# Kernel optimization log

Hardware: AMD Instinct MI355X
Metric: run time of the kernel (lower is better)

Reference implementation:

```python
import jax, jax.numpy as jnp
import numpy as np

N_NODES = 131072
IN_F = 512
HID = 512
H = 8
DH = HID // H
B = 1024  # batch_size (num graphs); static for jit
LN_EPS = 1e-5


def setup_inputs() -> dict:
    key = jax.random.key(0)
    ks = jax.random.split(key, 12)
    # equal-size segments (128 nodes/graph), sorted as in PyG batching
    batch = (jnp.arange(N_NODES) // (N_NODES // B)).astype(jnp.int32)
    s = 0.02
    return {
        "x": jax.random.normal(ks[0], (N_NODES, IN_F), jnp.float32),
        "batch": batch,
        "query": jax.random.normal(ks[1], (H, DH), jnp.float32) * s,
        "key_w": jax.random.normal(ks[2], (HID, IN_F), jnp.float32) * s,
        "key_b": jnp.zeros((HID,), jnp.float32),
        "value_w": jax.random.normal(ks[3], (HID, IN_F), jnp.float32) * s,
        "value_b": jnp.zeros((HID,), jnp.float32),
        "out_w": jax.random.normal(ks[4], (IN_F, HID), jnp.float32) * s,
        "out_b": jnp.zeros((IN_F,), jnp.float32),
        "gate_w": jax.random.normal(ks[5], (IN_F, 2 * IN_F), jnp.float32) * s,
        "gate_b": jnp.zeros((IN_F,), jnp.float32),
        "ln_w": jnp.ones((IN_F,), jnp.float32),
        "ln_b": jnp.zeros((IN_F,), jnp.float32),
    }


def reference(x, batch, query, key_w, key_b, value_w, value_b, out_w, out_b,
              gate_w, gate_b, ln_w, ln_b):
    N = x.shape[0]
    # projections (dense GEMMs)
    keys = (x @ key_w.T + key_b).reshape(N, H, DH)
    values = (x @ value_w.T + value_b).reshape(N, H, DH)
    # per-node attention logits against shared per-head query: [N, H]
    scores = jnp.einsum('nhd,hd->nh', keys, query)
    # segment softmax over nodes within each graph
    smax = jax.ops.segment_max(scores, batch, num_segments=B)  # [B, H]
    smax = jnp.where(jnp.isfinite(smax), smax, 0.0)            # guard empty graphs
    e = jnp.exp(scores - smax[batch])
    ssum = jax.ops.segment_sum(e, batch, num_segments=B)       # [B, H]
    w = e / jnp.maximum(ssum[batch], 1e-12)                    # [N, H]  (dropout is eval-mode identity)
    # attention-weighted pooling of values: [B, H, DH] -> [B, HID]
    pooled = jax.ops.segment_sum(w[:, :, None] * values, batch, num_segments=B)
    ctx = pooled.reshape(B, HID) @ out_w.T + out_b             # [B, IN_F]
    # gating with per-graph mean pool
    counts = jax.ops.segment_sum(jnp.ones((N,), x.dtype), batch, num_segments=B)
    avg = jax.ops.segment_sum(x, batch, num_segments=B) / jnp.maximum(counts, 1.0)[:, None]
    gate = jax.nn.sigmoid(jnp.concatenate([ctx, avg], axis=1) @ gate_w.T + gate_b)
    ctx = gate * ctx + (1.0 - gate) * avg
    emb = jnp.where(counts[:, None] > 0, ctx, 0.0)             # empty graphs stay zero
    # LayerNorm
    mu = emb.mean(-1, keepdims=True)
    var = emb.var(-1, keepdims=True)
    return (emb - mu) / jnp.sqrt(var + LN_EPS) * ln_w + ln_b
```

## Files before the change

### kernel.cpp

```cpp
#include <hip/hip_runtime.h>
#include <hip/hip_bf16.h>

typedef short short8 __attribute__((ext_vector_type(8)));
typedef float f32x4 __attribute__((ext_vector_type(4)));

#define NGRAPH 1024
#define NPG    128
#define INF    512
#define NHEAD  8

__device__ __forceinline__ ushort f2b(float f){
  __hip_bfloat16 h(f);
  union { __hip_bfloat16 h; ushort u; } v; v.h = h; return v.u;
}
__device__ __forceinline__ float b2f_lo(unsigned u){
  union { unsigned u; float f; } v; v.u = u << 16; return v.f;
}
__device__ __forceinline__ float b2f_hi(unsigned u){
  union { unsigned u; float f; } v; v.u = u & 0xffff0000u; return v.f;
}

__global__ void k_prep(const float* __restrict__ q, const float* __restrict__ kw,
                       float* __restrict__ kq,
                       const float* __restrict__ vw, ushort* __restrict__ vwb,
                       const float* __restrict__ ow, ushort* __restrict__ owb,
                       const float* __restrict__ gw, ushort* __restrict__ gwb){
  const int b = blockIdx.x, t = threadIdx.x;
  if(b < 16){
    int h = b >> 1, f = (b & 1)*256 + t;
    float s = 0.f;
    #pragma unroll 8
    for(int d = 0; d < 64; d++)
      s += q[h*64 + d] * kw[(size_t)(h*64 + d)*INF + f];
    kq[h*INF + f] = s;
  } else if(b < 16 + 1024){
    int i = (b - 16)*256 + t;   vwb[i] = f2b(vw[i]);
  } else if(b < 16 + 2048){
    int i = (b - 1040)*256 + t; owb[i] = f2b(ow[i]);
  } else {
    int i = (b - 2064)*256 + t; gwb[i] = f2b(gw[i]);
  }
}

__global__ __launch_bounds__(256, 2) void k_graph(
    const float* __restrict__ x, const float* __restrict__ kq,
    ushort* __restrict__ xw_b, float* __restrict__ avg_f, ushort* __restrict__ avg_b){
  __shared__ __align__(16) ushort xs[64*INF];
  __shared__ __align__(16) float  sc[64*NHEAD];
  __shared__ float mE[2*NHEAD];
  __shared__ float fD[2*NHEAD];

  const int t = threadIdx.x, lane = t & 63, w = t >> 6;
  const int col = lane & 15, kg = lane >> 4;
  const int g = blockIdx.x;
  const int node = w*16 + col;

  short8 bfrag[16];
  {
    const bool ok = (col < 8);
    const float* kqr = kq + col*INF;
    #pragma unroll
    for(int ks = 0; ks < 16; ks++){
      short8 v = short8{0,0,0,0,0,0,0,0};
      if(ok){
        float4 p0 = *(const float4*)(kqr + ks*32 + kg*8);
        float4 p1 = *(const float4*)(kqr + ks*32 + kg*8 + 4);
        v[0]=(short)f2b(p0.x); v[1]=(short)f2b(p0.y); v[2]=(short)f2b(p0.z); v[3]=(short)f2b(p0.w);
        v[4]=(short)f2b(p1.x); v[5]=(short)f2b(p1.y); v[6]=(short)f2b(p1.z); v[7]=(short)f2b(p1.w);
      }
      bfrag[ks] = v;
    }
  }

  float acc[2][NHEAD][2];
  #pragma unroll
  for(int c = 0; c < 2; c++)
    #pragma unroll
    for(int h = 0; h < NHEAD; h++){ acc[c][h][0] = 0.f; acc[c][h][1] = 0.f; }
  float cs0 = 0.f, cs1 = 0.f;

  #pragma unroll
  for(int c = 0; c < 2; c++){
    {
      const float* xr = x + (size_t)(g*NPG + c*64 + node)*INF + kg*8;
      f32x4 sacc = {0.f,0.f,0.f,0.f};
      #pragma unroll
      for(int ks = 0; ks < 16; ks++){
        float4 a = *(const float4*)(xr + ks*32);
        float4 b = *(const float4*)(xr + ks*32 + 4);
        short8 af;
        af[0]=(short)f2b(a.x); af[1]=(short)f2b(a.y); af[2]=(short)f2b(a.z); af[3]=(short)f2b(a.w);
        af[4]=(short)f2b(b.x); af[5]=(short)f2b(b.y); af[6]=(short)f2b(b.z); af[7]=(short)f2b(b.w);
        *(short8*)((char*)xs + node*1024 + ((ks*64 + kg*16) ^ ((node & 7) << 4))) = af;
        sacc = __builtin_amdgcn_mfma_f32_16x16x32_bf16(af, bfrag[ks], sacc, 0, 0, 0);
      }
      if(col < 8){
        #pragma unroll
        for(int r = 0; r < 4; r++)
          sc[(w*16 + kg*4 + r)*NHEAD + col] = sacc[r];
      }
    }
    __syncthreads();

    if(t < 128){
      int h = t >> 4, s = t & 15;
      float v[4]; float m = -1e30f;
      #pragma unroll
      for(int i = 0; i < 4; i++){ v[i] = sc[(s + 16*i)*NHEAD + h]; m = fmaxf(m, v[i]); }
      #pragma unroll
      for(int msk = 1; msk < 16; msk <<= 1) m = fmaxf(m, __shfl_xor(m, msk));
      float es = 0.f;
      #pragma unroll
      for(int i = 0; i < 4; i++){ v[i] = __expf(v[i] - m); es += v[i]; }
      #pragma unroll
      for(int msk = 1; msk < 16; msk <<= 1) es += __shfl_xor(es, msk);
      if(c == 0){
        #pragma unroll
        for(int i = 0; i < 4; i++) sc[(s + 16*i)*NHEAD + h] = v[i];
        if(s == 0){ mE[h] = m; mE[8 + h] = es; }
      } else {
        float m0 = mE[h], E0 = mE[8 + h];
        float M  = fmaxf(m0, m);
        float f1 = __expf(m - M);
        #pragma unroll
        for(int i = 0; i < 4; i++) sc[(s + 16*i)*NHEAD + h] = v[i]*f1;
        if(s == 0){
          float f0 = __expf(m0 - M);
          float D  = f0*E0 + f1*es;
          fD[h] = f0; fD[8 + h] = 1.0f / fmaxf(D, 1e-12f);
        }
      }
    }
    __syncthreads();

    #pragma unroll 4
    for(int n = 0; n < 64; n++){
      unsigned xv = *(const unsigned*)((const char*)xs + n*1024 + ((4*t) ^ ((n & 7) << 4)));
      float x0 = b2f_lo(xv), x1 = b2f_hi(xv);
      float4 w0 = *(float4*)(sc + n*NHEAD);
      float4 w1 = *(float4*)(sc + n*NHEAD + 4);
      float wv[8] = {w0.x, w0.y, w0.z, w0.w, w1.x, w1.y, w1.z, w1.w};
      #pragma unroll
      for(int h = 0; h < NHEAD; h++){
        acc[c][h][0] += wv[h]*x0;
        acc[c][h][1] += wv[h]*x1;
      }
      cs0 += x0; cs1 += x1;
    }
    __syncthreads();
  }

  #pragma unroll
  for(int h = 0; h < NHEAD; h++){
    float f0 = fD[h], dinv = fD[8 + h];
    float v0 = (f0*acc[0][h][0] + acc[1][h][0]) * dinv;
    float v1 = (f0*acc[0][h][1] + acc[1][h][1]) * dinv;
    unsigned pk = (unsigned)f2b(v0) | ((unsigned)f2b(v1) << 16);
    *(unsigned*)(xw_b + (size_t)g*4096 + h*INF + 2*t) = pk;
  }
  float am0 = cs0*(1.0f/128.0f), am1 = cs1*(1.0f/128.0f);
  float2 av = {am0, am1};
  *(float2*)(avg_f + (size_t)g*INF + 2*t) = av;
  unsigned pk = (unsigned)f2b(am0) | ((unsigned)f2b(am1) << 16);
  *(unsigned*)(avg_b + (size_t)g*INF + 2*t) = pk;
}

__global__ __launch_bounds__(256, 2) void gemm_tn(
    const ushort* __restrict__ A1, const ushort* __restrict__ A2,
    int lda, int headmode,
    const ushort* __restrict__ Wt, int ldw,
    const float* __restrict__ bias,
    float* __restrict__ Cf, ushort* __restrict__ Cb,
    int ldc, int K, int ksplit){
  __shared__ ushort As[2][64*40];
  __shared__ ushort Bs[2][64*40];
  const int t = threadIdx.x, lane = t & 63, w = t >> 6;
  const int m0 = blockIdx.x*64, n0 = blockIdx.y*64;
  const int aoff = headmode ? blockIdx.y*512 : 0;
  const int col = lane & 15, kg = lane >> 4;
  const int lr = t >> 2, lk = (t & 3)*8;

  f32x4 acc[2][2];
  #pragma unroll
  for(int i = 0; i < 2; i++)
    #pragma unroll
    for(int j = 0; j < 2; j++) acc[i][j] = f32x4{0.f,0.f,0.f,0.f};

  const ushort* Ap0 = (0 < ksplit) ? A1 : A2;
  short8 va = *(const short8*)(Ap0 + (size_t)(m0 + lr)*lda + aoff + lk);
  short8 vb = *(const short8*)(Wt + (size_t)(n0 + lr)*ldw + lk);
  int buf = 0;
  for(int kc = 0; kc < K; kc += 32){
    *(short8*)((char*)&As[buf][0] + lr*80 + lk*2) = va;
    *(short8*)((char*)&Bs[buf][0] + lr*80 + lk*2) = vb;
    __syncthreads();
    if(kc + 32 < K){
      int kn = kc + 32;
      const ushort* Ap = (kn < ksplit) ? A1 : A2;
      int kl = (kn < ksplit) ? kn : kn - ksplit;
      va = *(const short8*)(Ap + (size_t)(m0 + lr)*lda + aoff + kl + lk);
      vb = *(const short8*)(Wt + (size_t)(n0 + lr)*ldw + kn + lk);
    }
    const int mr = (w & 1)*32, nc = (w >> 1)*32;
    short8 af0 = *(short8*)((char*)&As[buf][0] + (mr + col)*80 + kg*16);
    short8 af1 = *(short8*)((char*)&As[buf][0] + (mr + 16 + col)*80 + kg*16);
    short8 bf0 = *(short8*)((char*)&Bs[buf][0] + (nc + col)*80 + kg*16);
    short8 bf1 = *(short8*)((char*)&Bs[buf][0] + (nc + 16 + col)*80 + kg*16);
    acc[0][0] = __builtin_amdgcn_mfma_f32_16x16x32_bf16(af0, bf0, acc[0][0], 0,0,0);
    acc[0][1] = __builtin_amdgcn_mfma_f32_16x16x32_bf16(af0, bf1, acc[0][1], 0,0,0);
    acc[1][0] = __builtin_amdgcn_mfma_f32_16x16x32_bf16(af1, bf0, acc[1][0], 0,0,0);
    acc[1][1] = __builtin_amdgcn_mfma_f32_16x16x32_bf16(af1, bf1, acc[1][1], 0,0,0);
    buf ^= 1;
  }
  #pragma unroll
  for(int mi = 0; mi < 2; mi++)
    #pragma unroll
    for(int ni = 0; ni < 2; ni++)
      #pragma unroll
      for(int r = 0; r < 4; r++){
        int rr = m0 + (w & 1)*32 + mi*16 + kg*4 + r;
        int cc = n0 + (w >> 1)*32 + ni*16 + col;
        float vv = acc[mi][ni][r] + bias[cc];
        if(Cf) Cf[(size_t)rr*ldc + cc] = vv;
        if(Cb) Cb[(size_t)rr*ldc + cc] = f2b(vv);
      }
}

__global__ __launch_bounds__(512, 2) void k5_epilogue(
    const float* __restrict__ z, const float* __restrict__ ctx,
    const float* __restrict__ avg, const float* __restrict__ lnw,
    const float* __restrict__ lnb, float* __restrict__ out){
  __shared__ float red[16];
  const int t = threadIdx.x, b = blockIdx.x;
  const size_t i = (size_t)b*INF + t;
  float zz = z[i], c = ctx[i], a = avg[i];
  float g = 1.0f / (1.0f + __expf(-zz));
  float e = g*c + (1.0f - g)*a;
  float s1 = e, s2 = e*e;
  #pragma unroll
  for(int m = 1; m < 64; m <<= 1){ s1 += __shfl_xor(s1, m); s2 += __shfl_xor(s2, m); }
  int wv = t >> 6;
  if((t & 63) == 0){ red[wv] = s1; red[8 + wv] = s2; }
  __syncthreads();
  float ts1 = 0.f, ts2 = 0.f;
  #pragma unroll
  for(int k = 0; k < 8; k++){ ts1 += red[k]; ts2 += red[8 + k]; }
  float mu = ts1 * (1.0f/512.0f);
  float var = ts2 * (1.0f/512.0f) - mu*mu;
  out[i] = (e - mu) * rsqrtf(var + 1e-5f) * lnw[t] + lnb[t];
}

extern "C" void kernel_launch(void* const* d_in, const int* in_sizes, int n_in,
                              void* d_out, int out_size, void* d_ws, size_t ws_size,
                              hipStream_t stream){
  const float* x       = (const float*)d_in[0];
  const float* query   = (const float*)d_in[2];
  const float* key_w   = (const float*)d_in[3];
  const float* value_w = (const float*)d_in[5];
  const float* value_b = (const float*)d_in[6];
  const float* out_w   = (const float*)d_in[7];
  const float* out_b   = (const float*)d_in[8];
  const float* gate_w  = (const float*)d_in[9];
  const float* gate_b  = (const float*)d_in[10];
  const float* ln_w    = (const float*)d_in[11];
  const float* ln_b    = (const float*)d_in[12];
  float* out = (float*)d_out;

  char* ws = (char*)d_ws;
  float*  kq       = (float*) (ws + 0);
  ushort* vw_b     = (ushort*)(ws + 16384);
  ushort* ow_b     = (ushort*)(ws + 540672);
  ushort* gw_b     = (ushort*)(ws + 1064960);
  ushort* xw_b     = (ushort*)(ws + 2113536);
  float*  avg_f    = (float*) (ws + 10502144);
  ushort* avg_b    = (ushort*)(ws + 12599296);
  ushort* pooled_b = (ushort*)(ws + 13647872);
  float*  ctx_f    = (float*) (ws + 14696448);
  ushort* ctx_b    = (ushort*)(ws + 16793600);
  float*  z_f      = (float*) (ws + 17842176);

  k_prep<<<4112, 256, 0, stream>>>(query, key_w, kq, value_w, vw_b,
                                   out_w, ow_b, gate_w, gw_b);

  k_graph<<<NGRAPH, 256, 0, stream>>>(x, kq, xw_b, avg_f, avg_b);

  gemm_tn<<<dim3(16, 8), 256, 0, stream>>>(xw_b, xw_b, 4096, 1, vw_b, 512, value_b,
                                           nullptr, pooled_b, 512, 512, 1 << 30);
  gemm_tn<<<dim3(16, 8), 256, 0, stream>>>(pooled_b, pooled_b, 512, 0, ow_b, 512, out_b,
                                           ctx_f, ctx_b, 512, 512, 1 << 30);
  gemm_tn<<<dim3(16, 8), 256, 0, stream>>>(ctx_b, avg_b, 512, 0, gw_b, 1024, gate_b,
                                           z_f, nullptr, 512, 1024, 512);

  k5_epilogue<<<NGRAPH, 512, 0, stream>>>(z_f, ctx_f, avg_f, ln_w, ln_b, out);
}
```

Measured before the change: 112.0 us.

## Shrink graph kernel to 128 threads with online softmax over 32-node chunks; deepen GEMM K-step

The per-graph kernel now runs 128 threads and walks the 128 nodes in four 32-node chunks. Its softmax becomes a running online rescale across chunks, so the shared staging buffer shrinks and more blocks can fit per CU. Each thread now accumulates four feature columns instead of two. Separately, the GEMM consumes 64 K-elements per shared-memory stage instead of 32, which halves the number of barriers. The trade-offs are more serial chunk iterations, fewer threads loading x per block, and higher register pressure.

```diff
diff --git a/kernel.cpp b/kernel.cpp
--- a/kernel.cpp
+++ b/kernel.cpp
@@ -8,6 +8,7 @@
 #define NPG    128
 #define INF    512
 #define NHEAD  8
+#define CH     32
 
 __device__ __forceinline__ ushort f2b(float f){
   __hip_bfloat16 h(f);
@@ -42,13 +43,12 @@
   }
 }
 
-__global__ __launch_bounds__(256, 2) void k_graph(
+__global__ __launch_bounds__(128, 2) void k_graph(
     const float* __restrict__ x, const float* __restrict__ kq,
     ushort* __restrict__ xw_b, float* __restrict__ avg_f, ushort* __restrict__ avg_b){
-  __shared__ __align__(16) ushort xs[64*INF];
-  __shared__ __align__(16) float  sc[64*NHEAD];
-  __shared__ float mE[2*NHEAD];
-  __shared__ float fD[2*NHEAD];
+  __shared__ __align__(16) ushort xs[CH*INF];
+  __shared__ __align__(16) float  sc[CH*NHEAD];
+  __shared__ float mEf[3*NHEAD];
 
   const int t = threadIdx.x, lane = t & 63, w = t >> 6;
   const int col = lane & 15, kg = lane >> 4;
@@ -72,17 +72,18 @@
     }
   }
 
-  float acc[2][NHEAD][2];
-  #pragma unroll
-  for(int c = 0; c < 2; c++)
-    #pragma unroll
-    for(int h = 0; h < NHEAD; h++){ acc[c][h][0] = 0.f; acc[c][h][1] = 0.f; }
-  float cs0 = 0.f, cs1 = 0.f;
-
-  #pragma unroll
-  for(int c = 0; c < 2; c++){
+  if(t < NHEAD){ mEf[t] = -1e30f; mEf[NHEAD + t] = 0.f; }
+
+  float acc[NHEAD][4];
+  #pragma unroll
+  for(int h = 0; h < NHEAD; h++)
+    #pragma unroll
+    for(int j = 0; j < 4; j++) acc[h][j] = 0.f;
+  float cs[4] = {0.f, 0.f, 0.f, 0.f};
+
+  for(int c = 0; c < 4; c++){
     {
-      const float* xr = x + (size_t)(g*NPG + c*64 + node)*INF + kg*8;
+      const float* xr = x + (size_t)(g*NPG + c*CH + node)*INF + kg*8;
       f32x4 sacc = {0.f,0.f,0.f,0.f};
       #pragma unroll
       for(int ks = 0; ks < 16; ks++){
@@ -102,67 +103,74 @@
     }
     __syncthreads();
 
-    if(t < 128){
+    {
       int h = t >> 4, s = t & 15;
-      float v[4]; float m = -1e30f;
-      #pragma unroll
-      for(int i = 0; i < 4; i++){ v[i] = sc[(s + 16*i)*NHEAD + h]; m = fmaxf(m, v[i]); }
+      float v[2]; float m = -1e30f;
+      #pragma unroll
+      for(int i = 0; i < 2; i++){ v[i] = sc[(s + 16*i)*NHEAD + h]; m = fmaxf(m, v[i]); }
       #pragma unroll
       for(int msk = 1; msk < 16; msk <<= 1) m = fmaxf(m, __shfl_xor(m, msk));
       float es = 0.f;
       #pragma unroll
-      for(int i = 0; i < 4; i++){ v[i] = __expf(v[i] - m); es += v[i]; }
+      for(int i = 0; i < 2; i++){ v[i] = __expf(v[i] - m); es += v[i]; }
       #pragma unroll
       for(int msk = 1; msk < 16; msk <<= 1) es += __shfl_xor(es, msk);
-      if(c == 0){
+      float M = mEf[h], E = mEf[NHEAD + h];
+      float Mn = fmaxf(M, m);
+      float f_old = __expf(M - Mn), f_new = __expf(m - Mn);
+      #pragma unroll
+      for(int i = 0; i < 2; i++) sc[(s + 16*i)*NHEAD + h] = v[i]*f_new;
+      if(s == 0){
+        mEf[h] = Mn;
+        mEf[NHEAD + h] = E*f_old + es*f_new;
+        mEf[2*NHEAD + h] = f_old;
+      }
+    }
+    __syncthreads();
+
+    {
+      float fo[NHEAD];
+      #pragma unroll
+      for(int h = 0; h < NHEAD; h++) fo[h] = mEf[2*NHEAD + h];
+      #pragma unroll
+      for(int h = 0; h < NHEAD; h++)
         #pragma unroll
-        for(int i = 0; i < 4; i++) sc[(s + 16*i)*NHEAD + h] = v[i];
-        if(s == 0){ mE[h] = m; mE[8 + h] = es; }
-      } else {
-        float m0 = mE[h], E0 = mE[8 + h];
-        float M  = fmaxf(m0, m);
-        float f1 = __expf(m - M);
+        for(int j = 0; j < 4; j++) acc[h][j] *= fo[h];
+      #pragma unroll 4
+      for(int n = 0; n < CH; n++){
+        uint2 xv = *(const uint2*)((const char*)xs + n*1024 + ((8*t) ^ ((n & 7) << 4)));
+        float x0 = b2f_lo(xv.x), x1 = b2f_hi(xv.x);
+        float x2 = b2f_lo(xv.y), x3 = b2f_hi(xv.y);
+        float4 w0 = *(float4*)(sc + n*NHEAD);
+        float4 w1 = *(float4*)(sc + n*NHEAD + 4);
+        float wv[8] = {w0.x, w0.y, w0.z, w0.w, w1.x, w1.y, w1.z, w1.w};
         #pragma unroll
-        for(int i = 0; i < 4; i++) sc[(s + 16*i)*NHEAD + h] = v[i]*f1;
-        if(s == 0){
-          float f0 = __expf(m0 - M);
-          float D  = f0*E0 + f1*es;
-          fD[h] = f0; fD[8 + h] = 1.0f / fmaxf(D, 1e-12f);
+        for(int h = 0; h < NHEAD; h++){
+          acc[h][0] += wv[h]*x0; acc[h][1] += wv[h]*x1;
+          acc[h][2] += wv[h]*x2; acc[h][3] += wv[h]*x3;
         }
+        cs[0] += x0; cs[1] += x1; cs[2] += x2; cs[3] += x3;
       }
     }
     __syncthreads();
-
-    #pragma unroll 4
-    for(int n = 0; n < 64; n++){
-      unsigned xv = *(const unsigned*)((const char*)xs + n*1024 + ((4*t) ^ ((n & 7) << 4)));
-      float x0 = b2f_lo(xv), x1 = b2f_hi(xv);
-      float4 w0 = *(float4*)(sc + n*NHEAD);
-      float4 w1 = *(float4*)(sc + n*NHEAD + 4);
-      float wv[8] = {w0.x, w0.y, w0.z, w0.w, w1.x, w1.y, w1.z, w1.w};
-      #pragma unroll
-      for(int h = 0; h < NHEAD; h++){
-        acc[c][h][0] += wv[h]*x0;
-        acc[c][h][1] += wv[h]*x1;
-      }
-      cs0 += x0; cs1 += x1;
-    }
-    __syncthreads();
   }
 
   #pragma unroll
   for(int h = 0; h < NHEAD; h++){
-    float f0 = fD[h], dinv = fD[8 + h];
-    float v0 = (f0*acc[0][h][0] + acc[1][h][0]) * dinv;
-    float v1 = (f0*acc[0][h][1] + acc[1][h][1]) * dinv;
-    unsigned pk = (unsigned)f2b(v0) | ((unsigned)f2b(v1) << 16);
-    *(unsigned*)(xw_b + (size_t)g*4096 + h*INF + 2*t) = pk;
-  }
-  float am0 = cs0*(1.0f/128.0f), am1 = cs1*(1.0f/128.0f);
-  float2 av = {am0, am1};
-  *(float2*)(avg_f + (size_t)g*INF + 2*t) = av;
-  unsigned pk = (unsigned)f2b(am0) | ((unsigned)f2b(am1) << 16);
-  *(unsigned*)(avg_b + (size_t)g*INF + 2*t) = pk;
+    float einv = 1.0f / fmaxf(mEf[NHEAD + h], 1e-12f);
+    float v0 = acc[h][0]*einv, v1 = acc[h][1]*einv;
+    float v2 = acc[h][2]*einv, v3 = acc[h][3]*einv;
+    uint2 pk = { (unsigned)f2b(v0) | ((unsigned)f2b(v1) << 16),
+                 (unsigned)f2b(v2) | ((unsigned)f2b(v3) << 16) };
+    *(uint2*)(xw_b + (size_t)g*4096 + h*INF + 4*t) = pk;
+  }
+  float am0 = cs[0]*(1.0f/128.0f), am1 = cs[1]*(1.0f/128.0f);
+  float am2 = cs[2]*(1.0f/128.0f), am3 = cs[3]*(1.0f/128.0f);
+  float4 av = {am0, am1, am2, am3};
+  *(float4*)(avg_f + (size_t)g*INF + 4*t) = av;
+  uint2 pk = { (unsigned)f2b(am0) | ((unsigned)f2b(am1) << 16),
+               (unsigned)f2b(am2) | ((unsigned)f2b(am3) << 16) };
+  *(uint2*)(avg_b + (size_t)g*INF + 4*t) = pk;
 }
 
 __global__ __launch_bounds__(256, 2) void gemm_tn(
@@ -172,13 +180,13 @@
     const float* __restrict__ bias,
     float* __restrict__ Cf, ushort* __restrict__ Cb,
     int ldc, int K, int ksplit){
-  __shared__ ushort As[2][64*40];
-  __shared__ ushort Bs[2][64*40];
+  __shared__ ushort As[2][64*72];
+  __shared__ ushort Bs[2][64*72];
   const int t = threadIdx.x, lane = t & 63, w = t >> 6;
   const int m0 = blockIdx.x*64, n0 = blockIdx.y*64;
   const int aoff = headmode ? blockIdx.y*512 : 0;
   const int col = lane & 15, kg = lane >> 4;
-  const int lr = t >> 2, lk = (t & 3)*8;
+  const int lr = t >> 2, lk = (t & 3)*16;
 
   f32x4 acc[2][2];
   #pragma unroll
@@ -187,29 +195,38 @@
     for(int j = 0; j < 2; j++) acc[i][j] = f32x4{0.f,0.f,0.f,0.f};
 
   const ushort* Ap0 = (0 < ksplit) ? A1 : A2;
-  short8 va = *(const short8*)(Ap0 + (size_t)(m0 + lr)*lda + aoff + lk);
-  short8 vb = *(const short8*)(Wt + (size_t)(n0 + lr)*ldw + lk);
+  short8 va0 = *(const short8*)(Ap0 + (size_t)(m0 + lr)*lda + aoff + lk);
+  short8 va1 = *(const short8*)(Ap0 + (size_t)(m0 + lr)*lda + aoff + lk + 8);
+  short8 vb0 = *(const short8*)(Wt + (size_t)(n0 + lr)*ldw + lk);
+  short8 vb1 = *(const short8*)(Wt + (size_t)(n0 + lr)*ldw + lk + 8);
   int buf = 0;
-  for(int kc = 0; kc < K; kc += 32){
-    *(short8*)((char*)&As[buf][0] + lr*80 + lk*2) = va;
-    *(short8*)((char*)&Bs[buf][0] + lr*80 + lk*2) = vb;
+  for(int kc = 0; kc < K; kc += 64){
+    *(short8*)((char*)&As[buf][0] + lr*144 + lk*2)      = va0;
+    *(short8*)((char*)&As[buf][0] + lr*144 + lk*2 + 16) = va1;
+    *(short8*)((char*)&Bs[buf][0] + lr*144 + lk*2)      = vb0;
+    *(short8*)((char*)&Bs[buf][0] + lr*144 + lk*2 + 16) = vb1;
     __syncthreads();
-    if(kc + 32 < K){
-      int kn = kc + 32;
+    if(kc + 64 < K){
+      int kn = kc + 64;
       const ushort* Ap = (kn < ksplit) ? A1 : A2;
       int kl = (kn < ksplit) ? kn : kn - ksplit;
-      va = *(const short8*)(Ap + (size_t)(m0 + lr)*lda + aoff + kl + lk);
-      vb = *(const short8*)(Wt + (size_t)(n0 + lr)*ldw + kn + lk);
+      va0 = *(const short8*)(Ap + (size_t)(m0 + lr)*lda + aoff + kl + lk);
+      va1 = *(const short8*)(Ap + (size_t)(m0 + lr)*lda + aoff + kl + lk + 8);
+      vb0 = *(const short8*)(Wt + (size_t)(n0 + lr)*ldw + kn + lk);
+      vb1 = *(const short8*)(Wt + (size_t)(n0 + lr)*ldw + kn + lk + 8);
     }
     const int mr = (w & 1)*32, nc = (w >> 1)*32;
-    short8 af0 = *(short8*)((char*)&As[buf][0] + (mr + col)*80 + kg*16);
-    short8 af1 = *(short8*)((char*)&As[buf][0] + (mr + 16 + col)*80 + kg*16);
-    short8 bf0 = *(short8*)((char*)&Bs[buf][0] + (nc + col)*80 + kg*16);
-    short8 bf1 = *(short8*)((char*)&Bs[buf][0] + (nc + 16 + col)*80 + kg*16);
-    acc[0][0] = __builtin_amdgcn_mfma_f32_16x16x32_bf16(af0, bf0, acc[0][0], 0,0,0);
-    acc[0][1] = __builtin_amdgcn_mfma_f32_16x16x32_bf16(af0, bf1, acc[0][1], 0,0,0);
-    acc[1][0] = __builtin_amdgcn_mfma_f32_16x16x32_bf16(af1, bf0, acc[1][0], 0,0,0);
-    acc[1][1] = __builtin_amdgcn_mfma_f32_16x16x32_bf16(af1, bf1, acc[1][1], 0,0,0);
+    #pragma unroll
+    for(int kk = 0; kk < 2; kk++){
+      short8 af0 = *(short8*)((char*)&As[buf][0] + (mr + col)*144      + kk*64 + kg*16);
+      short8 af1 = *(short8*)((char*)&As[buf][0] + (mr + 16 + col)*144 + kk*64 + kg*16);
+      short8 bf0 = *(short8*)((char*)&Bs[buf][0] + (nc + col)*144      + kk*64 + kg*16);
+      short8 bf1 = *(short8*)((char*)&Bs[buf][0] + (nc + 16 + col)*144 + kk*64 + kg*16);
+      acc[0][0] = __builtin_amdgcn_mfma_f32_16x16x32_bf16(af0, bf0, acc[0][0], 0,0,0);
+      acc[0][1] = __builtin_amdgcn_mfma_f32_16x16x32_bf16(af0, bf1, acc[0][1], 0,0,0);
+      acc[1][0] = __builtin_amdgcn_mfma_f32_16x16x32_bf16(af1, bf0, acc[1][0], 0,0,0);
+      acc[1][1] = __builtin_amdgcn_mfma_f32_16x16x32_bf16(af1, bf1, acc[1][1], 0,0,0);
+    }
     buf ^= 1;
   }
   #pragma unroll
@@ -282,7 +299,7 @@
   k_prep<<<4112, 256, 0, stream>>>(query, key_w, kq, value_w, vw_b,
                                    out_w, ow_b, gate_w, gw_b);
 
-  k_graph<<<NGRAPH, 256, 0, stream>>>(x, kq, xw_b, avg_f, avg_b);
+  k_graph<<<NGRAPH, 128, 0, stream>>>(x, kq, xw_b, avg_f, avg_b);
 
   gemm_tn<<<dim3(16, 8), 256, 0, stream>>>(xw_b, xw_b, 4096, 1, vw_b, 512, value_b,
                                            nullptr, pooled_b, 512, 512, 1 << 30);
```

New measurement: 97.34 us. 1.15x faster.
